# Kernel tuning notes

Measured on AMD Instinct MI355X. Metric: run time of the kernel, lower is better.

## Reference

```python
import jax, jax.numpy as jnp
import numpy as np

B, T, F_DIM = 32, 512, 128
HID, OUT, KS = 256, 4, 3
PAD_LEN = 512          # round(T * (200/stage_timepoints - 1)), stage_timepoints = 100
MMD_SIGMA = 1.0
DILATIONS = (1, 2, 4)  # config.dilation_expand = 2, num_layers = 3


def setup_inputs() -> dict:
    key = jax.random.key(0)
    keys = iter(jax.random.split(key, 40))
    s = 0.05

    def lin(o, i):
        return jax.random.normal(next(keys), (o, i), jnp.float32) * s

    def vec(o):
        return jnp.zeros((o,), jnp.float32)

    inp = {
        "feature1": jax.random.normal(next(keys), (B, F_DIM, 1, T), jnp.float32),
        "feature2": jax.random.normal(next(keys), (B, F_DIM, 1, T), jnp.float32),
    }
    # cross-attention params (A and B branches)
    for tag in ("a", "b"):
        for nm in ("q", "k", "v"):
            inp["w%s_%s" % (nm, tag)] = lin(F_DIM, F_DIM)
            inp["b%s_%s" % (nm, tag)] = vec(F_DIM)
    # TCN layers
    in_ch = F_DIM
    for i in range(3):
        inp["conv_w%d" % i] = jax.random.normal(next(keys), (HID, in_ch, KS), jnp.float32) * s
        inp["conv_b%d" % i] = vec(HID)
        inp["res_w%d" % i] = lin(HID, in_ch)
        inp["res_b%d" % i] = vec(HID)
        in_ch = HID
    inp["fc_w"] = lin(OUT, HID)
    inp["fc_b"] = vec(OUT)
    return inp


def _cross_attention(A, Bseq, wq, bq, wk, bk, wv, bv):
    # A, Bseq: [B, T, F]
    Q = A @ wq.T + bq
    K = Bseq @ wk.T + bk
    V = Bseq @ wv.T + bv
    scale = 1.0 / jnp.sqrt(jnp.asarray(Q.shape[-1], Q.dtype))
    scores = jnp.einsum('btf,bsf->bts', Q, K) * scale
    w = jax.nn.softmax(scores, axis=-1)
    return jnp.einsum('bts,bsf->btf', w, V)


def _tcn_layer(x, cw, cb, rw, rb, dilation):
    # x: [B, C, T]; causal left pad then dilated conv
    pad = (KS - 1) * dilation
    xp = jnp.pad(x, ((0, 0), (0, 0), (pad, 0)))
    out = jax.lax.conv_general_dilated(
        xp, cw, window_strides=(1,), padding='VALID',
        rhs_dilation=(dilation,), dimension_numbers=('NCH', 'OIH', 'NCH'))
    out = jax.nn.relu(out + cb[None, :, None])
    res = jnp.einsum('bct,oc->bot', x, rw) + rb[None, :, None]
    return out + res


def _pairwise_dist(x, y):
    # x, y: [B, T, F] -> [B, B, T]; ||x_i - y_j||^2 per time point via norm expansion
    sx = jnp.sum(x * x, axis=-1)  # [B, T]
    sy = jnp.sum(y * y, axis=-1)  # [B, T]
    return sx[:, None, :] + sy[None, :, :] - 2.0 * jnp.einsum('itf,jtf->ijt', x, y)


def _mmd_loss(f1, f2):
    inv = 1.0 / (2.0 * MMD_SIGMA ** 2)
    K_XX = jnp.exp(-_pairwise_dist(f1, f1) * inv)
    K_YY = jnp.exp(-_pairwise_dist(f2, f2) * inv)
    K_XY = jnp.exp(-_pairwise_dist(f1, f2) * inv)
    return jnp.mean(K_XX + K_YY - 2.0 * K_XY)


def reference(feature1, feature2,
              wq_a, bq_a, wk_a, bk_a, wv_a, bv_a,
              wq_b, bq_b, wk_b, bk_b, wv_b, bv_b,
              conv_w0, conv_b0, res_w0, res_b0,
              conv_w1, conv_b1, res_w1, res_b1,
              conv_w2, conv_b2, res_w2, res_b2,
              fc_w, fc_b):
    # [B, F, 1, T] -> [B, T, F]
    f1 = jnp.transpose(feature1[:, :, 0, :], (0, 2, 1))
    f2 = jnp.transpose(feature2[:, :, 0, :], (0, 2, 1))

    f1 = _cross_attention(f2, f1, wq_a, bq_a, wk_a, bk_a, wv_a, bv_a) * f1 + f1
    f2 = _cross_attention(f1, f2, wq_b, bq_b, wk_b, bk_b, wv_b, bv_b) * f2 + f2

    # temporal-offset padding: f1 padded right, f2 padded left, then summed
    p1 = jnp.pad(f1, ((0, 0), (0, PAD_LEN), (0, 0)))
    p2 = jnp.pad(f2, ((0, 0), (PAD_LEN, 0), (0, 0)))
    x = jnp.transpose(p1 + p2, (0, 2, 1))  # [B, F, T+PAD]

    tcn_params = ((conv_w0, conv_b0, res_w0, res_b0),
                  (conv_w1, conv_b1, res_w1, res_b1),
                  (conv_w2, conv_b2, res_w2, res_b2))
    for (cw, cb, rw, rb), d in zip(tcn_params, DILATIONS):
        x = _tcn_layer(x, cw, cb, rw, rb, d)

    pooled = jnp.mean(x, axis=2)          # [B, HID]
    output = pooled @ fc_w.T + fc_b       # [B, OUT]
    loss = _mmd_loss(f1, f2)
    return output, loss
```

## Files before the change

kernel.cpp:

```cpp
#include <hip/hip_runtime.h>

#define BB 32
#define TT 512
#define FF 128
#define HID 256
#define TP 1024

typedef __attribute__((ext_vector_type(8))) short s16x8;
typedef __attribute__((ext_vector_type(8))) unsigned short u16x8;
typedef __attribute__((ext_vector_type(4))) unsigned short u16x4;
typedef __attribute__((ext_vector_type(4))) float f32x4;

static __device__ __forceinline__ unsigned short f2bf(float f) {
    unsigned u = __builtin_bit_cast(unsigned, f);
    u = (u + 0x7FFFu + ((u >> 16) & 1u)) >> 16;
    return (unsigned short)u;
}
static __device__ __forceinline__ float bf2f(unsigned short b) {
    return __builtin_bit_cast(float, ((unsigned)b) << 16);
}

static __device__ __forceinline__ void tcnw_prep(
    int idx, const float* __restrict__ cw, const float* __restrict__ rw,
    unsigned short* __restrict__ out, int Cin)
{
    int p = idx / (256 * Cin);
    int rem = idx - p * 256 * Cin;
    int o = rem / Cin, c = rem - o * Cin;
    float v = (p < 3) ? cw[(o * Cin + c) * 3 + p] : rw[o * Cin + c];
    out[idx] = f2bf(v);
}

__global__ __launch_bounds__(256) void prep_all_kernel(
    const float* __restrict__ wqa, const float* __restrict__ wka,
    const float* __restrict__ wva, const float* __restrict__ wqb,
    const float* __restrict__ wkb, const float* __restrict__ wvb,
    const float* __restrict__ cw0, const float* __restrict__ rw0,
    const float* __restrict__ cw1, const float* __restrict__ rw1,
    const float* __restrict__ cw2, const float* __restrict__ rw2,
    unsigned short* __restrict__ qkvw, unsigned short* __restrict__ wb0,
    unsigned short* __restrict__ wb1, unsigned short* __restrict__ wb2)
{
    int idx = blockIdx.x * 256 + threadIdx.x;
    if (idx < 98304) {
        int p = idx >> 14, rc = idx & 16383;
        const float* srcs[6] = {wqa, wka, wva, wqb, wkb, wvb};
        float v = srcs[p][rc];
        if (p == 0 || p == 3) v *= 0.088388347648318447f;
        qkvw[idx] = f2bf(v);
    } else if (idx < 229376) {
        tcnw_prep(idx - 98304, cw0, rw0, wb0, 128);
    } else if (idx < 491520) {
        tcnw_prep(idx - 229376, cw1, rw1, wb1, 256);
    } else if (idx < 753664) {
        tcnw_prep(idx - 491520, cw2, rw2, wb2, 256);
    }
}

__global__ __launch_bounds__(256) void proj_mfma_kernel(
    const void* __restrict__ xq_src, int xq_mode, long long xq_bs,
    const void* __restrict__ xkv_src, int xkv_mode, long long xkv_bs,
    const unsigned short* __restrict__ w3,
    const float* __restrict__ bq, const float* __restrict__ bk,
    const float* __restrict__ bv,
    unsigned short* __restrict__ Qo, unsigned short* __restrict__ Ko,
    unsigned short* __restrict__ Vt)
{
    int t0 = blockIdx.x * 64, b = blockIdx.y;
    __shared__ __align__(16) unsigned short xsq[64 * 136];
    __shared__ __align__(16) unsigned short xskv[64 * 136];
    int tid = threadIdx.x;
    int wid = tid >> 6, lane = tid & 63;
    int n = lane & 15, g = lane >> 4;
    int tsub = (wid & 1) * 16, fh = (wid >> 1) * 64;

    if (xq_mode == 0) {
        const float* s = (const float*)xq_src + (size_t)b * xq_bs;
        for (int l = tid; l < 8192; l += 256) {
            int c = l >> 6, tt = l & 63;
            xsq[tt * 136 + c] = f2bf(s[(size_t)c * TT + t0 + tt]);
        }
    } else {
        const unsigned short* s = (const unsigned short*)xq_src + (size_t)b * xq_bs;
        for (int l = tid; l < 1024; l += 256) {
            int r = l >> 4, cc = l & 15;
            *(u16x8*)&xsq[r * 136 + cc * 8] = *(const u16x8*)&s[(size_t)(t0 + r) * FF + cc * 8];
        }
    }
    if (xkv_mode == 0) {
        const float* s = (const float*)xkv_src + (size_t)b * xkv_bs;
        for (int l = tid; l < 8192; l += 256) {
            int c = l >> 6, tt = l & 63;
            xskv[tt * 136 + c] = f2bf(s[(size_t)c * TT + t0 + tt]);
        }
    } else {
        const unsigned short* s = (const unsigned short*)xkv_src + (size_t)b * xkv_bs;
        for (int l = tid; l < 1024; l += 256) {
            int r = l >> 4, cc = l & 15;
            *(u16x8*)&xskv[r * 136 + cc * 8] = *(const u16x8*)&s[(size_t)(t0 + r) * FF + cc * 8];
        }
    }
    __syncthreads();

    f32x4 acc[2][3][4];
#pragma unroll
    for (int tt = 0; tt < 2; ++tt)
#pragma unroll
        for (int p = 0; p < 3; ++p)
#pragma unroll
            for (int i = 0; i < 4; ++i) acc[tt][p][i] = (f32x4){0.f, 0.f, 0.f, 0.f};

#pragma unroll
    for (int kk = 0; kk < 4; ++kk) {
        s16x8 bxq0 = *(const s16x8*)&xsq[(tsub + n) * 136 + kk * 32 + g * 8];
        s16x8 bxq1 = *(const s16x8*)&xsq[(32 + tsub + n) * 136 + kk * 32 + g * 8];
        s16x8 bxk0 = *(const s16x8*)&xskv[(tsub + n) * 136 + kk * 32 + g * 8];
        s16x8 bxk1 = *(const s16x8*)&xskv[(32 + tsub + n) * 136 + kk * 32 + g * 8];
#pragma unroll
        for (int i = 0; i < 4; ++i) {
            const unsigned short* wb = &w3[(size_t)(fh + i * 16 + n) * 128 + kk * 32 + g * 8];
            s16x8 a0 = *(const s16x8*)&wb[0];
            s16x8 a1 = *(const s16x8*)&wb[16384];
            s16x8 a2 = *(const s16x8*)&wb[32768];
            acc[0][0][i] = __builtin_amdgcn_mfma_f32_16x16x32_bf16(a0, bxq0, acc[0][0][i], 0, 0, 0);
            acc[0][1][i] = __builtin_amdgcn_mfma_f32_16x16x32_bf16(a1, bxk0, acc[0][1][i], 0, 0, 0);
            acc[0][2][i] = __builtin_amdgcn_mfma_f32_16x16x32_bf16(a2, bxk0, acc[0][2][i], 0, 0, 0);
            acc[1][0][i] = __builtin_amdgcn_mfma_f32_16x16x32_bf16(a0, bxq1, acc[1][0][i], 0, 0, 0);
            acc[1][1][i] = __builtin_amdgcn_mfma_f32_16x16x32_bf16(a1, bxk1, acc[1][1][i], 0, 0, 0);
            acc[1][2][i] = __builtin_amdgcn_mfma_f32_16x16x32_bf16(a2, bxk1, acc[1][2][i], 0, 0, 0);
        }
    }

    const float scale = 0.088388347648318447f;
#pragma unroll
    for (int tt = 0; tt < 2; ++tt) {
        int t = t0 + tt * 32 + tsub + n;
#pragma unroll
        for (int i = 0; i < 4; ++i) {
            int fb = fh + i * 16 + g * 4;
            u16x4 pk;
#pragma unroll
            for (int r = 0; r < 4; ++r) pk[r] = f2bf(acc[tt][0][i][r] + bq[fb + r] * scale);
            *(u16x4*)&Qo[((size_t)b * TT + t) * FF + fb] = pk;
#pragma unroll
            for (int r = 0; r < 4; ++r) pk[r] = f2bf(acc[tt][1][i][r] + bk[fb + r]);
            *(u16x4*)&Ko[((size_t)b * TT + t) * FF + fb] = pk;
#pragma unroll
            for (int r = 0; r < 4; ++r)
                Vt[((size_t)b * FF + fb + r) * TT + t] = f2bf(acc[tt][2][i][r] + bv[fb + r]);
        }
    }
}

__global__ __launch_bounds__(256) void attn_mfma_kernel(
    const unsigned short* __restrict__ Qb, const unsigned short* __restrict__ Kb,
    const unsigned short* __restrict__ Vtb,
    const float* __restrict__ orig, long long bso, int cso, int tso,
    float* __restrict__ out_tf, unsigned short* __restrict__ out_x, int xoff)
{
    __shared__ __align__(16) unsigned short Ks[64 * 136];
    __shared__ __align__(16) unsigned short Vs[128 * 72];
    __shared__ __align__(16) unsigned short Ps[4 * 16 * 68];

    int t0 = blockIdx.x * 64, b = blockIdx.y;
    int tid = threadIdx.x;
    int wid = tid >> 6, lane = tid & 63;
    int n = lane & 15, g = lane >> 4;
    int q0 = t0 + wid * 16;
    unsigned short* Pw = &Ps[wid * 1088];

    s16x8 qf[4];
#pragma unroll
    for (int kk = 0; kk < 4; ++kk)
        qf[kk] = *(const s16x8*)&Qb[((size_t)b * TT + q0 + n) * FF + kk * 32 + g * 8];

    u16x8 kst[4], vst[4];
#pragma unroll
    for (int ii = 0; ii < 4; ++ii) {
        int l = tid + 256 * ii;
        kst[ii] = *(const u16x8*)&Kb[((size_t)b * TT + (l >> 4)) * FF + (l & 15) * 8];
        vst[ii] = *(const u16x8*)&Vtb[((size_t)b * FF + (l >> 3)) * TT + (l & 7) * 8];
    }

    f32x4 O[8];
#pragma unroll
    for (int ft = 0; ft < 8; ++ft) O[ft] = (f32x4){0.f, 0.f, 0.f, 0.f};
    float m[4] = {-1e30f, -1e30f, -1e30f, -1e30f};
    float lsum[4] = {0.f, 0.f, 0.f, 0.f};

    for (int it = 0; it < 8; ++it) {
        __syncthreads();
#pragma unroll
        for (int ii = 0; ii < 4; ++ii) {
            int l = tid + 256 * ii;
            *(u16x8*)&Ks[(l >> 4) * 136 + (l & 15) * 8] = kst[ii];
            *(u16x8*)&Vs[(l >> 3) * 72 + (l & 7) * 8] = vst[ii];
        }
        __syncthreads();
        if (it < 7) {
            int s0n = (it + 1) * 64;
#pragma unroll
            for (int ii = 0; ii < 4; ++ii) {
                int l = tid + 256 * ii;
                kst[ii] = *(const u16x8*)&Kb[((size_t)b * TT + s0n + (l >> 4)) * FF + (l & 15) * 8];
                vst[ii] = *(const u16x8*)&Vtb[((size_t)b * FF + (l >> 3)) * TT + s0n + (l & 7) * 8];
            }
        }

        f32x4 acc[4];
#pragma unroll
        for (int st = 0; st < 4; ++st) acc[st] = (f32x4){0.f, 0.f, 0.f, 0.f};
        __builtin_amdgcn_s_setprio(1);
#pragma unroll
        for (int kk = 0; kk < 4; ++kk) {
#pragma unroll
            for (int st = 0; st < 4; ++st) {
                s16x8 kf = *(const s16x8*)&Ks[(st * 16 + n) * 136 + kk * 32 + g * 8];
                acc[st] = __builtin_amdgcn_mfma_f32_16x16x32_bf16(qf[kk], kf, acc[st], 0, 0, 0);
            }
        }
        __builtin_amdgcn_s_setprio(0);

        float mnew[4], c[4], rs[4];
#pragma unroll
        for (int r = 0; r < 4; ++r) {
            float tm = fmaxf(fmaxf(acc[0][r], acc[1][r]), fmaxf(acc[2][r], acc[3][r]));
#pragma unroll
            for (int msk = 1; msk < 16; msk <<= 1) tm = fmaxf(tm, __shfl_xor(tm, msk));
            mnew[r] = fmaxf(m[r], tm);
            c[r] = __expf(m[r] - mnew[r]);
            m[r] = mnew[r];
            rs[r] = 0.f;
        }
#pragma unroll
        for (int st = 0; st < 4; ++st) {
#pragma unroll
            for (int r = 0; r < 4; ++r) {
                float p = __expf(acc[st][r] - mnew[r]);
                rs[r] += p;
                Pw[(g * 4 + r) * 68 + st * 16 + n] = f2bf(p);
            }
        }
#pragma unroll
        for (int r = 0; r < 4; ++r) {
#pragma unroll
            for (int msk = 1; msk < 16; msk <<= 1) rs[r] += __shfl_xor(rs[r], msk);
            lsum[r] = lsum[r] * c[r] + rs[r];
        }
#pragma unroll
        for (int ft = 0; ft < 8; ++ft) {
#pragma unroll
            for (int r = 0; r < 4; ++r) O[ft][r] *= c[r];
        }

        __builtin_amdgcn_s_setprio(1);
#pragma unroll
        for (int ks = 0; ks < 2; ++ks) {
            s16x8 pf = *(const s16x8*)&Pw[n * 68 + ks * 32 + g * 8];
#pragma unroll
            for (int ft = 0; ft < 8; ++ft) {
                s16x8 vf = *(const s16x8*)&Vs[(ft * 16 + n) * 72 + ks * 32 + g * 8];
                O[ft] = __builtin_amdgcn_mfma_f32_16x16x32_bf16(pf, vf, O[ft], 0, 0, 0);
            }
        }
        __builtin_amdgcn_s_setprio(0);
    }

    float rinv[4];
#pragma unroll
    for (int r = 0; r < 4; ++r) rinv[r] = 1.f / lsum[r];
#pragma unroll
    for (int ft = 0; ft < 8; ++ft) {
        int f = ft * 16 + n;
#pragma unroll
        for (int r = 0; r < 4; ++r) {
            int q = q0 + g * 4 + r;
            float val = O[ft][r] * rinv[r];
            float xv = orig[bso * b + (size_t)f * cso + (size_t)q * tso];
            float res = val * xv + xv;
            out_tf[((size_t)b * TT + q) * FF + f] = res;
            out_x[((size_t)b * TP + xoff + q) * FF + f] = f2bf(res);
        }
    }
}

__global__ __launch_bounds__(256) void mmd_kernel(
    const float* __restrict__ f1, const float* __restrict__ f2,
    float* __restrict__ partials)
{
    int t = blockIdx.x;
    __shared__ __align__(16) unsigned short X1h[32 * 136], X1l[32 * 136];
    __shared__ __align__(16) unsigned short X2h[32 * 136], X2l[32 * 136];
    __shared__ float Gs[3][32][33];
    __shared__ float red[256];
    int tid = threadIdx.x;

    for (int l = tid; l < 4096; l += 256) {
        int i = l >> 7, f = l & 127;
        float v1 = f1[((size_t)i * TT + t) * FF + f];
        float v2 = f2[((size_t)i * TT + t) * FF + f];
        unsigned short h1 = f2bf(v1);
        unsigned short h2 = f2bf(v2);
        X1h[i * 136 + f] = h1;
        X1l[i * 136 + f] = f2bf(v1 - bf2f(h1));
        X2h[i * 136 + f] = h2;
        X2l[i * 136 + f] = f2bf(v2 - bf2f(h2));
    }
    __syncthreads();

    int wid = tid >> 6, lane = tid & 63;
    int n = lane & 15, g = lane >> 4;
#pragma unroll
    for (int uu = 0; uu < 3; ++uu) {
        int u = wid * 3 + uu;
        int gram = u >> 2, quad = u & 3;
        int qi = quad >> 1, qj = quad & 1;
        const unsigned short* Ah = (gram == 1) ? X2h : X1h;
        const unsigned short* Al = (gram == 1) ? X2l : X1l;
        const unsigned short* Bh = (gram == 0) ? X1h : X2h;
        const unsigned short* Bl = (gram == 0) ? X1l : X2l;
        f32x4 acc = (f32x4){0.f, 0.f, 0.f, 0.f};
#pragma unroll
        for (int kk = 0; kk < 4; ++kk) {
            int ao = (qi * 16 + n) * 136 + kk * 32 + g * 8;
            int bo = (qj * 16 + n) * 136 + kk * 32 + g * 8;
            s16x8 ah = *(const s16x8*)&Ah[ao];
            s16x8 al = *(const s16x8*)&Al[ao];
            s16x8 bh = *(const s16x8*)&Bh[bo];
            s16x8 bl = *(const s16x8*)&Bl[bo];
            acc = __builtin_amdgcn_mfma_f32_16x16x32_bf16(ah, bh, acc, 0, 0, 0);
            acc = __builtin_amdgcn_mfma_f32_16x16x32_bf16(ah, bl, acc, 0, 0, 0);
            acc = __builtin_amdgcn_mfma_f32_16x16x32_bf16(al, bh, acc, 0, 0, 0);
        }
#pragma unroll
        for (int r = 0; r < 4; ++r)
            Gs[gram][qi * 16 + g * 4 + r][qj * 16 + n] = acc[r];
    }
    __syncthreads();

    float s = 0.f;
#pragma unroll
    for (int r = 0; r < 4; ++r) {
        int p = tid + 256 * r;
        int i = p >> 5, j = p & 31;
        float d11 = Gs[0][i][i] + Gs[0][j][j] - 2.f * Gs[0][i][j];
        float d22 = Gs[1][i][i] + Gs[1][j][j] - 2.f * Gs[1][i][j];
        float d12 = Gs[0][i][i] + Gs[1][j][j] - 2.f * Gs[2][i][j];
        s += __expf(-0.5f * d11) + __expf(-0.5f * d22) - 2.f * __expf(-0.5f * d12);
    }
    red[tid] = s;
    __syncthreads();
    for (int off = 128; off; off >>= 1) {
        if (tid < off) red[tid] += red[tid + off];
        __syncthreads();
    }
    if (tid == 0) partials[t] = red[0];
}

__global__ __launch_bounds__(256, 2) void tcn_mfma_kernel(
    const unsigned short* __restrict__ x, int Cin, int d,
    const unsigned short* __restrict__ w4,
    const float* __restrict__ cb, const float* __restrict__ rb,
    unsigned short* __restrict__ out, float* __restrict__ pool_out, int do_pool)
{
    int t0 = blockIdx.x * 256, o0 = blockIdx.y * 64, b = blockIdx.z;
    __shared__ __align__(16) unsigned short smem[20800];
    __shared__ float pool_s[4][64];
    unsigned short* xs = smem;
    unsigned short* wsh = smem + 10560;
    int tid = threadIdx.x;
    int wid = tid >> 6, lane = tid & 63;
    int n = lane & 15, g = lane >> 4;
    int wt = wid * 64;
    int d2 = 2 * d;
    const unsigned short* xb = x + (size_t)b * TP * Cin;

    int gg = tid & 3;
    int xr0 = tid >> 2;
    int tg0 = t0 - d2 + xr0;
    bool xv4 = xr0 < d2;
    const unsigned short* wbase = w4 + (size_t)(o0 + (tid >> 2)) * Cin + gg * 8;
    size_t wps = (size_t)256 * Cin;

    u16x8 sx0, sx1, sx2, sx3, sx4, sw0, sw1, sw2, sw3;
    const u16x8 zz = {0, 0, 0, 0, 0, 0, 0, 0};
#define LDST(C0)                                                               \
    do {                                                                       \
        sx0 = (tg0 >= 0) ? *(const u16x8*)&xb[(size_t)tg0 * Cin + (C0) + gg * 8] : zz; \
        sx1 = *(const u16x8*)&xb[(size_t)(tg0 + 64) * Cin + (C0) + gg * 8];    \
        sx2 = *(const u16x8*)&xb[(size_t)(tg0 + 128) * Cin + (C0) + gg * 8];   \
        sx3 = *(const u16x8*)&xb[(size_t)(tg0 + 192) * Cin + (C0) + gg * 8];   \
        sx4 = xv4 ? *(const u16x8*)&xb[(size_t)(tg0 + 256) * Cin + (C0) + gg * 8] : zz; \
        sw0 = *(const u16x8*)&wbase[(C0)];                                     \
        sw1 = *(const u16x8*)&wbase[wps + (C0)];                               \
        sw2 = *(const u16x8*)&wbase[2 * wps + (C0)];                           \
        sw3 = *(const u16x8*)&wbase[3 * wps + (C0)];                           \
    } while (0)

    f32x4 accc[4][4], accr[4][4];
#pragma unroll
    for (int i = 0; i < 4; ++i)
#pragma unroll
        for (int j = 0; j < 4; ++j) {
            accc[i][j] = (f32x4){0.f, 0.f, 0.f, 0.f};
            accr[i][j] = (f32x4){0.f, 0.f, 0.f, 0.f};
        }

    LDST(0);
    for (int c0 = 0; c0 < Cin; c0 += 32) {
        __syncthreads();
        *(u16x8*)&xs[xr0 * 40 + gg * 8] = sx0;
        *(u16x8*)&xs[(xr0 + 64) * 40 + gg * 8] = sx1;
        *(u16x8*)&xs[(xr0 + 128) * 40 + gg * 8] = sx2;
        *(u16x8*)&xs[(xr0 + 192) * 40 + gg * 8] = sx3;
        if (xv4) *(u16x8*)&xs[(xr0 + 256) * 40 + gg * 8] = sx4;
        {
            int wrow = (tid >> 2) * 40 + gg * 8;
            *(u16x8*)&wsh[wrow] = sw0;
            *(u16x8*)&wsh[2560 + wrow] = sw1;
            *(u16x8*)&wsh[5120 + wrow] = sw2;
            *(u16x8*)&wsh[7680 + wrow] = sw3;
        }
        __syncthreads();
        if (c0 + 32 < Cin) LDST(c0 + 32);

        s16x8 bfr[4][3];
#pragma unroll
        for (int j = 0; j < 4; ++j) {
            int tl = wt + j * 16 + n;
#pragma unroll
            for (int k = 0; k < 3; ++k)
                bfr[j][k] = *(const s16x8*)&xs[(tl + k * d) * 40 + g * 8];
        }
        __builtin_amdgcn_s_setprio(1);
#pragma unroll
        for (int i = 0; i < 4; ++i) {
            int wrow = (i * 16 + n) * 40 + g * 8;
            s16x8 a0 = *(const s16x8*)&wsh[wrow];
            s16x8 a1 = *(const s16x8*)&wsh[2560 + wrow];
            s16x8 a2 = *(const s16x8*)&wsh[5120 + wrow];
            s16x8 ar = *(const s16x8*)&wsh[7680 + wrow];
#pragma unroll
            for (int j = 0; j < 4; ++j) {
                accc[i][j] = __builtin_amdgcn_mfma_f32_16x16x32_bf16(a0, bfr[j][0], accc[i][j], 0, 0, 0);
                accc[i][j] = __builtin_amdgcn_mfma_f32_16x16x32_bf16(a1, bfr[j][1], accc[i][j], 0, 0, 0);
                accc[i][j] = __builtin_amdgcn_mfma_f32_16x16x32_bf16(a2, bfr[j][2], accc[i][j], 0, 0, 0);
                accr[i][j] = __builtin_amdgcn_mfma_f32_16x16x32_bf16(ar, bfr[j][2], accr[i][j], 0, 0, 0);
            }
        }
        __builtin_amdgcn_s_setprio(0);
    }
#undef LDST

    if (!do_pool) {
        __syncthreads();
        unsigned short* ot = smem;
#pragma unroll
        for (int i = 0; i < 4; ++i) {
            int ob = o0 + i * 16 + g * 4;
            float cbv0 = cb[ob], cbv1 = cb[ob + 1], cbv2 = cb[ob + 2], cbv3 = cb[ob + 3];
            float rbv0 = rb[ob], rbv1 = rb[ob + 1], rbv2 = rb[ob + 2], rbv3 = rb[ob + 3];
#pragma unroll
            for (int j = 0; j < 4; ++j) {
                int tl = wt + j * 16 + n;
                u16x4 pk;
                pk[0] = f2bf(fmaxf(accc[i][j][0] + cbv0, 0.f) + accr[i][j][0] + rbv0);
                pk[1] = f2bf(fmaxf(accc[i][j][1] + cbv1, 0.f) + accr[i][j][1] + rbv1);
                pk[2] = f2bf(fmaxf(accc[i][j][2] + cbv2, 0.f) + accr[i][j][2] + rbv2);
                pk[3] = f2bf(fmaxf(accc[i][j][3] + cbv3, 0.f) + accr[i][j][3] + rbv3);
                *(u16x4*)&ot[tl * 66 + i * 16 + g * 4] = pk;
            }
        }
        __syncthreads();
        int tl = tid >> 3, c8 = tid & 7;
#pragma unroll
        for (int s = 0; s < 8; ++s) {
            int trow = tl + 32 * s;
            *(u16x8*)&out[((size_t)b * TP + t0 + trow) * HID + o0 + c8 * 8] =
                *(const u16x8*)&ot[trow * 66 + c8 * 8];
        }
    } else {
#pragma unroll
        for (int i = 0; i < 4; ++i) {
            int ob = o0 + i * 16 + g * 4;
            float cbv0 = cb[ob], cbv1 = cb[ob + 1], cbv2 = cb[ob + 2], cbv3 = cb[ob + 3];
            float rbv0 = rb[ob], rbv1 = rb[ob + 1], rbv2 = rb[ob + 2], rbv3 = rb[ob + 3];
            float ps0 = 0.f, ps1 = 0.f, ps2 = 0.f, ps3 = 0.f;
#pragma unroll
            for (int j = 0; j < 4; ++j) {
                ps0 += fmaxf(accc[i][j][0] + cbv0, 0.f) + accr[i][j][0] + rbv0;
                ps1 += fmaxf(accc[i][j][1] + cbv1, 0.f) + accr[i][j][1] + rbv1;
                ps2 += fmaxf(accc[i][j][2] + cbv2, 0.f) + accr[i][j][2] + rbv2;
                ps3 += fmaxf(accc[i][j][3] + cbv3, 0.f) + accr[i][j][3] + rbv3;
            }
#pragma unroll
            for (int msk = 1; msk < 16; msk <<= 1) {
                ps0 += __shfl_xor(ps0, msk);
                ps1 += __shfl_xor(ps1, msk);
                ps2 += __shfl_xor(ps2, msk);
                ps3 += __shfl_xor(ps3, msk);
            }
            if (n == 0) {
                int ol = i * 16 + g * 4;
                pool_s[wid][ol + 0] = ps0;
                pool_s[wid][ol + 1] = ps1;
                pool_s[wid][ol + 2] = ps2;
                pool_s[wid][ol + 3] = ps3;
            }
        }
        __syncthreads();
        if (tid < 64) {
            float s = pool_s[0][tid] + pool_s[1][tid] + pool_s[2][tid] + pool_s[3][tid];
            pool_out[((size_t)b * 4 + blockIdx.x) * HID + o0 + tid] = s;
        }
    }
}

__global__ __launch_bounds__(256) void final_kernel(
    const float* __restrict__ pp, const float* __restrict__ fcw,
    const float* __restrict__ fcb, const float* __restrict__ partials,
    float* __restrict__ dout)
{
    int tid = threadIdx.x;
    if (tid < 128) {
        int b = tid >> 2, k = tid & 3;
        float s = 0.f;
        for (int c = 0; c < HID; ++c) {
            float pc = 0.f;
#pragma unroll
            for (int xs = 0; xs < 4; ++xs) pc += pp[((size_t)b * 4 + xs) * HID + c];
            s += pc * fcw[k * HID + c];
        }
        dout[tid] = fcb[k] + s * (1.f / 1024.f);
    } else if (tid < 192) {
        int lane = tid - 128;
        float s = 0.f;
        for (int j = 0; j < 8; ++j) s += partials[lane + 64 * j];
        for (int off = 32; off; off >>= 1) s += __shfl_down(s, off);
        if (lane == 0) dout[128] = s * (1.f / (32.f * 32.f * 512.f));
    }
}

extern "C" void kernel_launch(void* const* d_in, const int* in_sizes, int n_in,
                              void* d_out, int out_size, void* d_ws, size_t ws_size,
                              hipStream_t stream)
{
    const float* feat1 = (const float*)d_in[0];
    const float* feat2 = (const float*)d_in[1];
    const float* wq_a = (const float*)d_in[2];
    const float* bq_a = (const float*)d_in[3];
    const float* wk_a = (const float*)d_in[4];
    const float* bk_a = (const float*)d_in[5];
    const float* wv_a = (const float*)d_in[6];
    const float* bv_a = (const float*)d_in[7];
    const float* wq_b = (const float*)d_in[8];
    const float* bq_b = (const float*)d_in[9];
    const float* wk_b = (const float*)d_in[10];
    const float* bk_b = (const float*)d_in[11];
    const float* wv_b = (const float*)d_in[12];
    const float* bv_b = (const float*)d_in[13];
    const float* cw0 = (const float*)d_in[14];
    const float* cb0 = (const float*)d_in[15];
    const float* rw0 = (const float*)d_in[16];
    const float* rb0 = (const float*)d_in[17];
    const float* cw1 = (const float*)d_in[18];
    const float* cb1 = (const float*)d_in[19];
    const float* rw1 = (const float*)d_in[20];
    const float* rb1 = (const float*)d_in[21];
    const float* cw2 = (const float*)d_in[22];
    const float* cb2 = (const float*)d_in[23];
    const float* rw2 = (const float*)d_in[24];
    const float* rb2 = (const float*)d_in[25];
    const float* fcw = (const float*)d_in[26];
    const float* fcb = (const float*)d_in[27];
    float* dout = (float*)d_out;

    float* ws = (float*)d_ws;
    unsigned short* Qbf = (unsigned short*)ws;
    unsigned short* Kbf = (unsigned short*)(ws + 1048576);
    unsigned short* Vt  = (unsigned short*)(ws + 2097152);
    float* f1tf = ws + 3145728;
    float* f2tf = ws + 5242880;
    unsigned short* xbuf = (unsigned short*)(ws + 7340032);
    unsigned short* wbuf = (unsigned short*)(ws + 9437184);
    unsigned short* wb0 = wbuf;
    unsigned short* wb1 = wbuf + 131072;
    unsigned short* wb2 = wbuf + 393216;
    unsigned short* qkvw = (unsigned short*)(ws + 9764864);
    unsigned short* w3a = qkvw;
    unsigned short* w3b = qkvw + 3 * 16384;
    float* poolpart = ws + 9814016;
    float* mmdpart  = ws + 9846784;
    unsigned short* h_a = (unsigned short*)ws;
    unsigned short* h_b = (unsigned short*)(ws + 4194304);

    prep_all_kernel<<<dim3(2944), 256, 0, stream>>>(
        wq_a, wk_a, wv_a, wq_b, wk_b, wv_b,
        cw0, rw0, cw1, rw1, cw2, rw2, qkvw, wb0, wb1, wb2);

    proj_mfma_kernel<<<dim3(8, 32), 256, 0, stream>>>(
        feat2, 0, 65536LL, feat1, 0, 65536LL, w3a,
        bq_a, bk_a, bv_a, Qbf, Kbf, Vt);
    attn_mfma_kernel<<<dim3(8, 32), 256, 0, stream>>>(
        Qbf, Kbf, Vt, feat1, 65536LL, 512, 1, f1tf, xbuf, 0);

    proj_mfma_kernel<<<dim3(8, 32), 256, 0, stream>>>(
        xbuf, 1, (long long)TP * FF, feat2, 0, 65536LL, w3b,
        bq_b, bk_b, bv_b, Qbf, Kbf, Vt);
    attn_mfma_kernel<<<dim3(8, 32), 256, 0, stream>>>(
        Qbf, Kbf, Vt, feat2, 65536LL, 512, 1, f2tf, xbuf, 512);

    mmd_kernel<<<dim3(512), 256, 0, stream>>>(f1tf, f2tf, mmdpart);

    tcn_mfma_kernel<<<dim3(4, 4, 32), 256, 0, stream>>>(xbuf, 128, 1, wb0, cb0, rb0, h_a, nullptr, 0);
    tcn_mfma_kernel<<<dim3(4, 4, 32), 256, 0, stream>>>(h_a, 256, 2, wb1, cb1, rb1, h_b, nullptr, 0);
    tcn_mfma_kernel<<<dim3(4, 4, 32), 256, 0, stream>>>(h_b, 256, 4, wb2, cb2, rb2, h_a, poolpart, 1);

    final_kernel<<<dim3(1), 256, 0, stream>>>(poolpart, fcw, fcb, mmdpart, dout);
}
```

Baseline: 173.9 us.

## Fold TCN weight prep into attention and MMD into first TCN launch

TCN weight conversion moves out of the prep kernel and into an extra row of blocks on the second attention launch. The MMD computation moves into an extra grid row of the first TCN layer, with each of those 128 blocks handling four timepoints. This removes two kernel launches and lets these small independent jobs share a launch with larger kernels, reducing idle tails. The cost is that h_a moves to a new workspace offset, and the MMD blocks run serially over four timepoints, which may lengthen the first TCN launch.

```diff
diff --git a/kernel.cpp b/kernel.cpp
--- a/kernel.cpp
+++ b/kernel.cpp
@@ -18,6 +18,21 @@
 }
 static __device__ __forceinline__ float bf2f(unsigned short b) {
     return __builtin_bit_cast(float, ((unsigned)b) << 16);
+}
+
+__global__ __launch_bounds__(256) void prep_qkvw_kernel(
+    const float* __restrict__ wqa, const float* __restrict__ wka,
+    const float* __restrict__ wva, const float* __restrict__ wqb,
+    const float* __restrict__ wkb, const float* __restrict__ wvb,
+    unsigned short* __restrict__ qkvw)
+{
+    int idx = blockIdx.x * 256 + threadIdx.x;
+    if (idx >= 98304) return;
+    int p = idx >> 14, rc = idx & 16383;
+    const float* srcs[6] = {wqa, wka, wva, wqb, wkb, wvb};
+    float v = srcs[p][rc];
+    if (p == 0 || p == 3) v *= 0.088388347648318447f;
+    qkvw[idx] = f2bf(v);
 }
 
 static __device__ __forceinline__ void tcnw_prep(
@@ -29,32 +44,6 @@
     int o = rem / Cin, c = rem - o * Cin;
     float v = (p < 3) ? cw[(o * Cin + c) * 3 + p] : rw[o * Cin + c];
     out[idx] = f2bf(v);
-}
-
-__global__ __launch_bounds__(256) void prep_all_kernel(
-    const float* __restrict__ wqa, const float* __restrict__ wka,
-    const float* __restrict__ wva, const float* __restrict__ wqb,
-    const float* __restrict__ wkb, const float* __restrict__ wvb,
-    const float* __restrict__ cw0, const float* __restrict__ rw0,
-    const float* __restrict__ cw1, const float* __restrict__ rw1,
-    const float* __restrict__ cw2, const float* __restrict__ rw2,
-    unsigned short* __restrict__ qkvw, unsigned short* __restrict__ wb0,
-    unsigned short* __restrict__ wb1, unsigned short* __restrict__ wb2)
-{
-    int idx = blockIdx.x * 256 + threadIdx.x;
-    if (idx < 98304) {
-        int p = idx >> 14, rc = idx & 16383;
-        const float* srcs[6] = {wqa, wka, wva, wqb, wkb, wvb};
-        float v = srcs[p][rc];
-        if (p == 0 || p == 3) v *= 0.088388347648318447f;
-        qkvw[idx] = f2bf(v);
-    } else if (idx < 229376) {
-        tcnw_prep(idx - 98304, cw0, rw0, wb0, 128);
-    } else if (idx < 491520) {
-        tcnw_prep(idx - 229376, cw1, rw1, wb1, 256);
-    } else if (idx < 753664) {
-        tcnw_prep(idx - 491520, cw2, rw2, wb2, 256);
-    }
 }
 
 __global__ __launch_bounds__(256) void proj_mfma_kernel(
@@ -156,14 +145,29 @@
     const unsigned short* __restrict__ Qb, const unsigned short* __restrict__ Kb,
     const unsigned short* __restrict__ Vtb,
     const float* __restrict__ orig, long long bso, int cso, int tso,
-    float* __restrict__ out_tf, unsigned short* __restrict__ out_x, int xoff)
+    float* __restrict__ out_tf, unsigned short* __restrict__ out_x, int xoff,
+    const float* __restrict__ cw0, const float* __restrict__ rw0,
+    const float* __restrict__ cw1, const float* __restrict__ rw1,
+    const float* __restrict__ cw2, const float* __restrict__ rw2,
+    unsigned short* __restrict__ wb0, unsigned short* __restrict__ wb1,
+    unsigned short* __restrict__ wb2)
 {
     __shared__ __align__(16) unsigned short Ks[64 * 136];
     __shared__ __align__(16) unsigned short Vs[128 * 72];
     __shared__ __align__(16) unsigned short Ps[4 * 16 * 68];
 
+    int tid = threadIdx.x;
+    if (blockIdx.y == 32) {
+        int idx0 = blockIdx.x * 256 + tid;
+        for (int idx = idx0; idx < 655360; idx += 2048) {
+            if (idx < 131072) tcnw_prep(idx, cw0, rw0, wb0, 128);
+            else if (idx < 393216) tcnw_prep(idx - 131072, cw1, rw1, wb1, 256);
+            else tcnw_prep(idx - 393216, cw2, rw2, wb2, 256);
+        }
+        return;
+    }
+
     int t0 = blockIdx.x * 64, b = blockIdx.y;
-    int tid = threadIdx.x;
     int wid = tid >> 6, lane = tid & 63;
     int n = lane & 15, g = lane >> 4;
     int q0 = t0 + wid * 16;
@@ -284,91 +288,105 @@
     }
 }
 
-__global__ __launch_bounds__(256) void mmd_kernel(
-    const float* __restrict__ f1, const float* __restrict__ f2,
-    float* __restrict__ partials)
-{
-    int t = blockIdx.x;
-    __shared__ __align__(16) unsigned short X1h[32 * 136], X1l[32 * 136];
-    __shared__ __align__(16) unsigned short X2h[32 * 136], X2l[32 * 136];
-    __shared__ float Gs[3][32][33];
-    __shared__ float red[256];
-    int tid = threadIdx.x;
-
-    for (int l = tid; l < 4096; l += 256) {
-        int i = l >> 7, f = l & 127;
-        float v1 = f1[((size_t)i * TT + t) * FF + f];
-        float v2 = f2[((size_t)i * TT + t) * FF + f];
-        unsigned short h1 = f2bf(v1);
-        unsigned short h2 = f2bf(v2);
-        X1h[i * 136 + f] = h1;
-        X1l[i * 136 + f] = f2bf(v1 - bf2f(h1));
-        X2h[i * 136 + f] = h2;
-        X2l[i * 136 + f] = f2bf(v2 - bf2f(h2));
-    }
-    __syncthreads();
-
-    int wid = tid >> 6, lane = tid & 63;
-    int n = lane & 15, g = lane >> 4;
-#pragma unroll
-    for (int uu = 0; uu < 3; ++uu) {
-        int u = wid * 3 + uu;
-        int gram = u >> 2, quad = u & 3;
-        int qi = quad >> 1, qj = quad & 1;
-        const unsigned short* Ah = (gram == 1) ? X2h : X1h;
-        const unsigned short* Al = (gram == 1) ? X2l : X1l;
-        const unsigned short* Bh = (gram == 0) ? X1h : X2h;
-        const unsigned short* Bl = (gram == 0) ? X1l : X2l;
-        f32x4 acc = (f32x4){0.f, 0.f, 0.f, 0.f};
-#pragma unroll
-        for (int kk = 0; kk < 4; ++kk) {
-            int ao = (qi * 16 + n) * 136 + kk * 32 + g * 8;
-            int bo = (qj * 16 + n) * 136 + kk * 32 + g * 8;
-            s16x8 ah = *(const s16x8*)&Ah[ao];
-            s16x8 al = *(const s16x8*)&Al[ao];
-            s16x8 bh = *(const s16x8*)&Bh[bo];
-            s16x8 bl = *(const s16x8*)&Bl[bo];
-            acc = __builtin_amdgcn_mfma_f32_16x16x32_bf16(ah, bh, acc, 0, 0, 0);
-            acc = __builtin_amdgcn_mfma_f32_16x16x32_bf16(ah, bl, acc, 0, 0, 0);
-            acc = __builtin_amdgcn_mfma_f32_16x16x32_bf16(al, bh, acc, 0, 0, 0);
-        }
-#pragma unroll
-        for (int r = 0; r < 4; ++r)
-            Gs[gram][qi * 16 + g * 4 + r][qj * 16 + n] = acc[r];
-    }
-    __syncthreads();
-
-    float s = 0.f;
-#pragma unroll
-    for (int r = 0; r < 4; ++r) {
-        int p = tid + 256 * r;
-        int i = p >> 5, j = p & 31;
-        float d11 = Gs[0][i][i] + Gs[0][j][j] - 2.f * Gs[0][i][j];
-        float d22 = Gs[1][i][i] + Gs[1][j][j] - 2.f * Gs[1][i][j];
-        float d12 = Gs[0][i][i] + Gs[1][j][j] - 2.f * Gs[2][i][j];
-        s += __expf(-0.5f * d11) + __expf(-0.5f * d22) - 2.f * __expf(-0.5f * d12);
-    }
-    red[tid] = s;
-    __syncthreads();
-    for (int off = 128; off; off >>= 1) {
-        if (tid < off) red[tid] += red[tid + off];
-        __syncthreads();
-    }
-    if (tid == 0) partials[t] = red[0];
-}
-
 __global__ __launch_bounds__(256, 2) void tcn_mfma_kernel(
     const unsigned short* __restrict__ x, int Cin, int d,
     const unsigned short* __restrict__ w4,
     const float* __restrict__ cb, const float* __restrict__ rb,
-    unsigned short* __restrict__ out, float* __restrict__ pool_out, int do_pool)
+    unsigned short* __restrict__ out, float* __restrict__ pool_out, int do_pool,
+    const float* __restrict__ f1, const float* __restrict__ f2,
+    float* __restrict__ partials, int do_mmd)
 {
-    int t0 = blockIdx.x * 256, o0 = blockIdx.y * 64, b = blockIdx.z;
     __shared__ __align__(16) unsigned short smem[20800];
     __shared__ float pool_s[4][64];
+    int tid = threadIdx.x;
+
+    if (do_mmd && blockIdx.y == 4) {
+        unsigned short* X1h = smem;
+        unsigned short* X1l = smem + 4352;
+        unsigned short* X2h = smem + 8704;
+        unsigned short* X2l = smem + 13056;
+        float* Gsf = (float*)smem;
+        float* red = Gsf + 3168;
+        int wid2 = tid >> 6, lane = tid & 63;
+        int n = lane & 15, g = lane >> 4;
+        int tb = (blockIdx.z * 4 + blockIdx.x) * 4;
+        for (int k4 = 0; k4 < 4; ++k4) {
+            int t = tb + k4;
+            __syncthreads();
+            for (int l = tid; l < 4096; l += 256) {
+                int i = l >> 7, f = l & 127;
+                float v1 = f1[((size_t)i * TT + t) * FF + f];
+                float v2 = f2[((size_t)i * TT + t) * FF + f];
+                unsigned short h1 = f2bf(v1);
+                unsigned short h2 = f2bf(v2);
+                X1h[i * 136 + f] = h1;
+                X1l[i * 136 + f] = f2bf(v1 - bf2f(h1));
+                X2h[i * 136 + f] = h2;
+                X2l[i * 136 + f] = f2bf(v2 - bf2f(h2));
+            }
+            __syncthreads();
+            f32x4 accu[3];
+#pragma unroll
+            for (int uu = 0; uu < 3; ++uu) {
+                int u = wid2 * 3 + uu;
+                int gram = u >> 2, quad = u & 3;
+                int qi = quad >> 1, qj = quad & 1;
+                const unsigned short* Ah = (gram == 1) ? X2h : X1h;
+                const unsigned short* Al = (gram == 1) ? X2l : X1l;
+                const unsigned short* Bh = (gram == 0) ? X1h : X2h;
+                const unsigned short* Bl = (gram == 0) ? X1l : X2l;
+                f32x4 acc = (f32x4){0.f, 0.f, 0.f, 0.f};
+#pragma unroll
+                for (int kk = 0; kk < 4; ++kk) {
+                    int ao = (qi * 16 + n) * 136 + kk * 32 + g * 8;
+                    int bo = (qj * 16 + n) * 136 + kk * 32 + g * 8;
+                    s16x8 ah = *(const s16x8*)&Ah[ao];
+                    s16x8 al = *(const s16x8*)&Al[ao];
+                    s16x8 bh = *(const s16x8*)&Bh[bo];
+                    s16x8 bl = *(const s16x8*)&Bl[bo];
+                    acc = __builtin_amdgcn_mfma_f32_16x16x32_bf16(ah, bh, acc, 0, 0, 0);
+                    acc = __builtin_amdgcn_mfma_f32_16x16x32_bf16(ah, bl, acc, 0, 0, 0);
+                    acc = __builtin_amdgcn_mfma_f32_16x16x32_bf16(al, bh, acc, 0, 0, 0);
+                }
+                accu[uu] = acc;
+            }
+            __syncthreads();
+#pragma unroll
+            for (int uu = 0; uu < 3; ++uu) {
+                int u = wid2 * 3 + uu;
+                int gram = u >> 2, quad = u & 3;
+                int qi = quad >> 1, qj = quad & 1;
+#pragma unroll
+                for (int r = 0; r < 4; ++r)
+                    Gsf[gram * 1056 + (qi * 16 + g * 4 + r) * 33 + qj * 16 + n] = accu[uu][r];
+            }
+            __syncthreads();
+            float s = 0.f;
+#pragma unroll
+            for (int r = 0; r < 4; ++r) {
+                int p = tid + 256 * r;
+                int i = p >> 5, j = p & 31;
+                float g11 = Gsf[i * 33 + i], g1jj = Gsf[j * 33 + j];
+                float g22 = Gsf[1056 + i * 33 + i], g2jj = Gsf[1056 + j * 33 + j];
+                float d11 = g11 + g1jj - 2.f * Gsf[i * 33 + j];
+                float d22 = g22 + g2jj - 2.f * Gsf[1056 + i * 33 + j];
+                float d12 = g11 + g2jj - 2.f * Gsf[2112 + i * 33 + j];
+                s += __expf(-0.5f * d11) + __expf(-0.5f * d22) - 2.f * __expf(-0.5f * d12);
+            }
+            red[tid] = s;
+            __syncthreads();
+            for (int off = 128; off; off >>= 1) {
+                if (tid < off) red[tid] += red[tid + off];
+                __syncthreads();
+            }
+            if (tid == 0) partials[t] = red[0];
+        }
+        return;
+    }
+
+    int t0 = blockIdx.x * 256, o0 = blockIdx.y * 64, b = blockIdx.z;
     unsigned short* xs = smem;
     unsigned short* wsh = smem + 10560;
-    int tid = threadIdx.x;
     int wid = tid >> 6, lane = tid & 63;
     int n = lane & 15, g = lane >> 4;
     int wt = wid * 64;
@@ -591,30 +609,32 @@
     unsigned short* w3b = qkvw + 3 * 16384;
     float* poolpart = ws + 9814016;
     float* mmdpart  = ws + 9846784;
-    unsigned short* h_a = (unsigned short*)ws;
+    unsigned short* h_a = (unsigned short*)(ws + 10485760);
     unsigned short* h_b = (unsigned short*)(ws + 4194304);
 
-    prep_all_kernel<<<dim3(2944), 256, 0, stream>>>(
-        wq_a, wk_a, wv_a, wq_b, wk_b, wv_b,
-        cw0, rw0, cw1, rw1, cw2, rw2, qkvw, wb0, wb1, wb2);
+    prep_qkvw_kernel<<<dim3(384), 256, 0, stream>>>(
+        wq_a, wk_a, wv_a, wq_b, wk_b, wv_b, qkvw);
 
     proj_mfma_kernel<<<dim3(8, 32), 256, 0, stream>>>(
         feat2, 0, 65536LL, feat1, 0, 65536LL, w3a,
         bq_a, bk_a, bv_a, Qbf, Kbf, Vt);
     attn_mfma_kernel<<<dim3(8, 32), 256, 0, stream>>>(
-        Qbf, Kbf, Vt, feat1, 65536LL, 512, 1, f1tf, xbuf, 0);
+        Qbf, Kbf, Vt, feat1, 65536LL, 512, 1, f1tf, xbuf, 0,
+        cw0, rw0, cw1, rw1, cw2, rw2, wb0, wb1, wb2);
 
     proj_mfma_kernel<<<dim3(8, 32), 256, 0, stream>>>(
         xbuf, 1, (long long)TP * FF, feat2, 0, 65536LL, w3b,
         bq_b, bk_b, bv_b, Qbf, Kbf, Vt);
-    attn_mfma_kernel<<<dim3(8, 32), 256, 0, stream>>>(
-        Qbf, Kbf, Vt, feat2, 65536LL, 512, 1, f2tf, xbuf, 512);
-
-    mmd_kernel<<<dim3(512), 256, 0, stream>>>(f1tf, f2tf, mmdpart);
-
-    tcn_mfma_kernel<<<dim3(4, 4, 32), 256, 0, stream>>>(xbuf, 128, 1, wb0, cb0, rb0, h_a, nullptr, 0);
-    tcn_mfma_kernel<<<dim3(4, 4, 32), 256, 0, stream>>>(h_a, 256, 2, wb1, cb1, rb1, h_b, nullptr, 0);
-    tcn_mfma_kernel<<<dim3(4, 4, 32), 256, 0, stream>>>(h_b, 256, 4, wb2, cb2, rb2, h_a, poolpart, 1);
+    attn_mfma_kernel<<<dim3(8, 33), 256, 0, stream>>>(
+        Qbf, Kbf, Vt, feat2, 65536LL, 512, 1, f2tf, xbuf, 512,
+        cw0, rw0, cw1, rw1, cw2, rw2, wb0, wb1, wb2);
+
+    tcn_mfma_kernel<<<dim3(4, 5, 32), 256, 0, stream>>>(
+        xbuf, 128, 1, wb0, cb0, rb0, h_a, nullptr, 0, f1tf, f2tf, mmdpart, 1);
+    tcn_mfma_kernel<<<dim3(4, 4, 32), 256, 0, stream>>>(
+        h_a, 256, 2, wb1, cb1, rb1, h_b, nullptr, 0, nullptr, nullptr, nullptr, 0);
+    tcn_mfma_kernel<<<dim3(4, 4, 32), 256, 0, stream>>>(
+        h_b, 256, 4, wb2, cb2, rb2, h_a, poolpart, 1, nullptr, nullptr, nullptr, 0);
 
     final_kernel<<<dim3(1), 256, 0, stream>>>(poolpart, fcw, fcb, mmdpart, dout);
 }
```

After: 279.5 us. 1.61x slower.
